# Kernel optimization log

Measured on AMD Instinct MI355X. Metric: run time of the kernel, lower is better.

## Reference

```python
import jax, jax.numpy as jnp
import numpy as np

B, L, C = 8, 4096, 1024
M = 16384  # memory bank size


def setup_inputs() -> dict:
    key = jax.random.key(0)
    k_f, k_w1, k_w2, k_mb = jax.random.split(key, 4)
    features = jax.random.normal(k_f, (B, L, C), dtype=jnp.float32)
    # Linear weights stored as (in, out); math identical to torch's x @ W.T + b.
    W1 = jax.random.normal(k_w1, (C, C // 2), dtype=jnp.float32) / np.sqrt(C)
    b1 = jnp.zeros((C // 2,), dtype=jnp.float32)
    W2 = jax.random.normal(k_w2, (C // 2, C // 4), dtype=jnp.float32) / np.sqrt(C // 2)
    b2 = jnp.zeros((C // 4,), dtype=jnp.float32)
    memory_bank = jax.random.normal(k_mb, (M, C // 4), dtype=jnp.float32)
    return {"features": features, "W1": W1, "b1": b1, "W2": W2, "b2": b2,
            "memory_bank": memory_bank}


def reference(features, W1, b1, W2, b2, memory_bank):
    # projection MLP: Linear -> ReLU -> Linear
    h = jax.nn.relu(jnp.einsum('blc,cd->bld', features, W1) + b1)
    proj = jnp.einsum('bld,de->ble', h, W2) + b2          # [B, L, D], D = C//4
    # Euclidean cdist against memory bank, then min over bank entries.
    x2 = jnp.sum(proj * proj, axis=-1, keepdims=True)      # [B, L, 1]
    m2 = jnp.sum(memory_bank * memory_bank, axis=-1)       # [M]
    xm = jnp.einsum('ble,me->blm', proj, memory_bank)      # [B, L, M]
    d2 = jnp.maximum(x2 - 2.0 * xm + m2, 0.0)
    dist = jnp.sqrt(d2)                                    # torch.cdist, p=2
    return jnp.min(dist, axis=-1)                          # [B, L]
```

## Files before the change

### kernel.cpp

```cpp
#include <hip/hip_runtime.h>
#include <math.h>

typedef __bf16 bf16;
typedef __attribute__((ext_vector_type(8))) __bf16 bf16x8;
typedef __attribute__((ext_vector_type(4))) float f32x4;
typedef __attribute__((ext_vector_type(8))) int i32x8;

typedef __attribute__((address_space(1))) const void gvoid;
typedef __attribute__((address_space(3))) void lvoid;
#define GLL(g, l) __builtin_amdgcn_global_load_lds((gvoid*)(g), (lvoid*)(l), 16, 0, 0)
#define MFMA(a, b, c) __builtin_amdgcn_mfma_f32_16x16x32_bf16((a), (b), (c), 0, 0, 0)
#define MFMAS(a, b, c) \
  __builtin_amdgcn_mfma_scale_f32_16x16x128_f8f6f4((a), (b), (c), 0, 0, 0, 0x7F, 0, 0x7F)

__device__ __forceinline__ int swz128(int row, int kb) { return kb ^ ((row & 7) << 4); }

__device__ __forceinline__ unsigned char f32_to_e4m3(float x) {
  const unsigned s = (__float_as_uint(x) >> 24) & 0x80;
  float ax = fminf(fabsf(x), 448.f);
  unsigned e;
  if (ax >= 0.015625f) {
    const unsigned u = __float_as_uint(ax);
    const unsigned t = u + 0x7FFFF + ((u >> 20) & 1);
    e = (((t >> 23) - 120) << 3) | ((t >> 20) & 7);
  } else {
    e = (unsigned)__float2int_rn(ax * 512.f);
  }
  return (unsigned char)(s | e);
}
__device__ __forceinline__ float e4m3_to_f32(unsigned char b) {
  const unsigned s = ((unsigned)b & 0x80) << 24;
  const unsigned em = b & 0x7F;
  float v;
  if (em >= 8) v = __uint_as_float((((em >> 3) + 120) << 23) | ((em & 7) << 20));
  else v = (float)em * 0.001953125f;
  return __uint_as_float(__float_as_uint(v) | s);
}

__global__ __launch_bounds__(256) void prep_w(const float* __restrict__ W1,
                                              const float* __restrict__ W2,
                                              bf16* __restrict__ W1t, bf16* __restrict__ W2t) {
  const int t = blockIdx.x * 256 + threadIdx.x;
  if (t < 512 * 1024) {
    const int h = t & 511, k = t >> 9;
    W1t[h * 1024 + k] = (bf16)W1[k * 512 + h];
  } else {
    const int u = t - 512 * 1024;
    const int e = u & 255, k = u >> 8;
    W2t[e * 512 + k] = (bf16)W2[k * 256 + e];
  }
}

__global__ __launch_bounds__(256) void prep_bank(const float* __restrict__ bank,
                                                 unsigned char* __restrict__ SB8,
                                                 float* __restrict__ m2) {
  const int tid = threadIdx.x, lane = tid & 63, wv = tid >> 6;
  const int row = blockIdx.x * 4 + wv;
  const float4 v = *reinterpret_cast<const float4*>(bank + (size_t)row * 256 + lane * 4);
  uchar4 q;
  float ssum = 0.f;
  {
    const float xs[4] = {v.x, v.y, v.z, v.w};
    unsigned char qb[4];
#pragma unroll
    for (int e = 0; e < 4; ++e) {
      qb[e] = f32_to_e4m3(-2.f * xs[e]);
      const float d = e4m3_to_f32(qb[e]);
      ssum += d * d;
    }
    q.x = qb[0]; q.y = qb[1]; q.z = qb[2]; q.w = qb[3];
  }
#pragma unroll
  for (int off = 1; off < 64; off <<= 1) ssum += __shfl_xor(ssum, off);
  const int t = row >> 7, ww = (row >> 4) & 7, lrr = row & 15;
  const int h = lane >> 5, lk = (lane >> 3) & 3, off32 = (lane & 7) * 4;
  const size_t dst = ((((size_t)t * 8 + ww) * 2 + h) * 64 + lk * 16 + lrr) * 32 + off32;
  *reinterpret_cast<uchar4*>(SB8 + dst) = q;
  if (lane == 0) m2[row] = ssum * 0.25f;
}

__global__ __launch_bounds__(512, 2) void mlp1_kernel(const float* __restrict__ F,
                                                      const bf16* __restrict__ W1t,
                                                      const float* __restrict__ b1,
                                                      bf16* __restrict__ H) {
  __shared__ __align__(16) char smem[81920];
  char* sA = smem;
  char* sB = smem + 16384;

  const int tid = threadIdx.x;
  const int w = tid >> 6, lane = tid & 63;
  const int wm = w >> 2, wn = w & 3;
  const int lr = lane & 15, lk = lane >> 4;
  const size_t r0 = (size_t)blockIdx.x * 128;

  f32x4 acc[4][8];
  const f32x4 z = {0.f, 0.f, 0.f, 0.f};
#pragma unroll
  for (int m = 0; m < 4; ++m)
#pragma unroll
    for (int n = 0; n < 8; ++n) acc[m][n] = z;

  for (int kc = 0; kc < 16; ++kc) {
    {
      const int fr = tid >> 2, kg = (tid & 3) << 4;
      const float* fsrc = F + (r0 + fr) * 1024 + kc * 64 + kg;
      const float4 f0 = *reinterpret_cast<const float4*>(fsrc);
      const float4 f1 = *reinterpret_cast<const float4*>(fsrc + 4);
      const float4 f2 = *reinterpret_cast<const float4*>(fsrc + 8);
      const float4 f3 = *reinterpret_cast<const float4*>(fsrc + 12);
      bf16x8 p0, p1;
      p0[0] = (bf16)f0.x; p0[1] = (bf16)f0.y; p0[2] = (bf16)f0.z; p0[3] = (bf16)f0.w;
      p0[4] = (bf16)f1.x; p0[5] = (bf16)f1.y; p0[6] = (bf16)f1.z; p0[7] = (bf16)f1.w;
      p1[0] = (bf16)f2.x; p1[1] = (bf16)f2.y; p1[2] = (bf16)f2.z; p1[3] = (bf16)f2.w;
      p1[4] = (bf16)f3.x; p1[5] = (bf16)f3.y; p1[6] = (bf16)f3.z; p1[7] = (bf16)f3.w;
      const int bb = kg * 2;
      *(bf16x8*)(sA + fr * 128 + swz128(fr, bb)) = p0;
      *(bf16x8*)(sA + fr * 128 + swz128(fr, bb + 16)) = p1;
    }
#pragma unroll
    for (int i = 0; i < 8; ++i) {
      const int o = (w * 8 + i) * 1024 + lane * 16;
      const int n = o >> 7, b = o & 127;
      GLL((const char*)W1t + n * 2048 + kc * 128 + swz128(n, b), sB + (w * 8 + i) * 1024);
    }
    __syncthreads();
#pragma unroll
    for (int ks = 0; ks < 2; ++ks) {
      bf16x8 av[4];
#pragma unroll
      for (int Mt = 0; Mt < 4; ++Mt) {
        const int row = wm * 64 + Mt * 16 + lr;
        av[Mt] = *(const bf16x8*)(sA + row * 128 + swz128(row, ks * 64 + lk * 16));
      }
#pragma unroll
      for (int Nt = 0; Nt < 8; ++Nt) {
        const int n = wn * 128 + Nt * 16 + lr;
        const bf16x8 bv = *(const bf16x8*)(sB + n * 128 + swz128(n, ks * 64 + lk * 16));
#pragma unroll
        for (int Mt = 0; Mt < 4; ++Mt) acc[Mt][Nt] = MFMA(av[Mt], bv, acc[Mt][Nt]);
      }
    }
    __syncthreads();
  }
#pragma unroll
  for (int Nt = 0; Nt < 8; ++Nt) {
    const int col = wn * 128 + Nt * 16 + lr;
    const float bias = b1[col];
#pragma unroll
    for (int Mt = 0; Mt < 4; ++Mt) {
      const size_t rowb = r0 + wm * 64 + Mt * 16 + lk * 4;
#pragma unroll
      for (int q = 0; q < 4; ++q)
        H[(rowb + q) * 512 + col] = (bf16)fmaxf(acc[Mt][Nt][q] + bias, 0.f);
    }
  }
}

__global__ __launch_bounds__(512, 2) void mlp2_kernel(const bf16* __restrict__ H,
                                                      const bf16* __restrict__ W2t,
                                                      const float* __restrict__ b2,
                                                      unsigned char* __restrict__ PROJ8,
                                                      float* __restrict__ X2) {
  __shared__ __align__(16) char smem[51200];
  char* sA = smem;
  char* sB = smem + 16384;
  float* sX2 = (float*)(smem + 49152);

  const int tid = threadIdx.x;
  const int w = tid >> 6, lane = tid & 63;
  const int wm = w >> 2, wn = w & 3;
  const int lr = lane & 15, lk = lane >> 4;
  const size_t r0 = (size_t)blockIdx.x * 128;

  f32x4 acc[4][4];
  const f32x4 z = {0.f, 0.f, 0.f, 0.f};
#pragma unroll
  for (int m = 0; m < 4; ++m)
#pragma unroll
    for (int n = 0; n < 4; ++n) acc[m][n] = z;

  for (int kc = 0; kc < 8; ++kc) {
#pragma unroll
    for (int i = 0; i < 2; ++i) {
      const int o = (w * 2 + i) * 1024 + lane * 16;
      const int row = o >> 7, b = o & 127;
      GLL((const char*)H + (r0 + row) * 1024 + kc * 128 + swz128(row, b), sA + (w * 2 + i) * 1024);
    }
#pragma unroll
    for (int i = 0; i < 4; ++i) {
      const int o = (w * 4 + i) * 1024 + lane * 16;
      const int n = o >> 7, b = o & 127;
      GLL((const char*)W2t + n * 1024 + kc * 128 + swz128(n, b), sB + (w * 4 + i) * 1024);
    }
    __syncthreads();
#pragma unroll
    for (int ks = 0; ks < 2; ++ks) {
      bf16x8 av[4];
#pragma unroll
      for (int Mt = 0; Mt < 4; ++Mt) {
        const int row = wm * 64 + Mt * 16 + lr;
        av[Mt] = *(const bf16x8*)(sA + row * 128 + swz128(row, ks * 64 + lk * 16));
      }
#pragma unroll
      for (int Nt = 0; Nt < 4; ++Nt) {
        const int n = wn * 64 + Nt * 16 + lr;
        const bf16x8 bv = *(const bf16x8*)(sB + n * 128 + swz128(n, ks * 64 + lk * 16));
#pragma unroll
        for (int Mt = 0; Mt < 4; ++Mt) acc[Mt][Nt] = MFMA(av[Mt], bv, acc[Mt][Nt]);
      }
    }
    __syncthreads();
  }
  float x2p[4][4];
#pragma unroll
  for (int m = 0; m < 4; ++m)
#pragma unroll
    for (int q = 0; q < 4; ++q) x2p[m][q] = 0.f;
#pragma unroll
  for (int Nt = 0; Nt < 4; ++Nt) {
    const int col = wn * 64 + Nt * 16 + lr;
    const float bias = b2[col];
#pragma unroll
    for (int Mt = 0; Mt < 4; ++Mt) {
      const size_t rowb = r0 + wm * 64 + Mt * 16 + lk * 4;
#pragma unroll
      for (int q = 0; q < 4; ++q) {
        const float p = acc[Mt][Nt][q] + bias;
        const unsigned char qb = f32_to_e4m3(p);
        PROJ8[(rowb + q) * 256 + col] = qb;
        const float d = e4m3_to_f32(qb);
        x2p[Mt][q] += d * d;
      }
    }
  }
#pragma unroll
  for (int Mt = 0; Mt < 4; ++Mt)
#pragma unroll
    for (int q = 0; q < 4; ++q) {
      float v = x2p[Mt][q];
      v += __shfl_xor(v, 1); v += __shfl_xor(v, 2);
      v += __shfl_xor(v, 4); v += __shfl_xor(v, 8);
      x2p[Mt][q] = v;
    }
  __syncthreads();
  if (lr == 0) {
#pragma unroll
    for (int Mt = 0; Mt < 4; ++Mt)
#pragma unroll
      for (int q = 0; q < 4; ++q)
        sX2[wn * 128 + wm * 64 + Mt * 16 + lk * 4 + q] = x2p[Mt][q];
  }
  __syncthreads();
  if (tid < 128)
    X2[r0 + tid] = sX2[tid] + sX2[128 + tid] + sX2[256 + tid] + sX2[384 + tid];
}

__global__ __launch_bounds__(512, 2) void dist_kernel(const unsigned char* __restrict__ PROJ8,
                                                      const unsigned char* __restrict__ SB8,
                                                      const float* __restrict__ m2g,
                                                      const float* __restrict__ X2,
                                                      float* __restrict__ out) {
  __shared__ float minbuf[1024];

  const int tid = threadIdx.x;
  const int w = tid >> 6, lane = tid & 63;
  const int lr = lane & 15, lk = lane >> 4;
  const size_t r0 = (size_t)blockIdx.x * 128;

  i32x8 A[8][2];
#pragma unroll
  for (int Mt = 0; Mt < 8; ++Mt)
#pragma unroll
    for (int h = 0; h < 2; ++h)
      A[Mt][h] = *(const i32x8*)(PROJ8 + (r0 + Mt * 16 + lr) * 256 + h * 128 + lk * 32);

  const char* sb = (const char*)SB8 + ((size_t)w * 2 * 64 + lane) * 32;
  const float* m2p = m2g + w * 16 + lr;

  f32x4 minv[8];
#pragma unroll
  for (int Mt = 0; Mt < 8; ++Mt)
#pragma unroll
    for (int q = 0; q < 4; ++q) minv[Mt][q] = 3.0e38f;

#define LOADT(B0, B1, MC, tt)                                \
  do {                                                       \
    B0 = *(const i32x8*)(sb + (size_t)(tt) * 32768);         \
    B1 = *(const i32x8*)(sb + (size_t)(tt) * 32768 + 2048);  \
    MC = m2p[(tt) * 128];                                    \
  } while (0)

#define COMPUTE(B0, B1, MC)                                                       \
  do {                                                                            \
    f32x4 mv;                                                                     \
    mv[0] = (MC); mv[1] = (MC); mv[2] = (MC); mv[3] = (MC);                       \
    f32x4 acc[8];                                                                 \
    __builtin_amdgcn_s_setprio(1);                                                \
    _Pragma("unroll") for (int Mt = 0; Mt < 8; ++Mt)                              \
      acc[Mt] = MFMAS(A[Mt][0], (B0), mv);                                        \
    _Pragma("unroll") for (int Mt = 0; Mt < 8; ++Mt)                              \
      acc[Mt] = MFMAS(A[Mt][1], (B1), acc[Mt]);                                   \
    __builtin_amdgcn_s_setprio(0);                                                \
    _Pragma("unroll") for (int Mt = 0; Mt < 8; ++Mt) {                            \
      minv[Mt][0] = fminf(minv[Mt][0], acc[Mt][0]);                               \
      minv[Mt][1] = fminf(minv[Mt][1], acc[Mt][1]);                               \
      minv[Mt][2] = fminf(minv[Mt][2], acc[Mt][2]);                               \
      minv[Mt][3] = fminf(minv[Mt][3], acc[Mt][3]);                               \
    }                                                                             \
  } while (0)

  i32x8 a0, a1, b0, b1;
  float ma, mb;
  LOADT(a0, a1, ma, 0);
  LOADT(b0, b1, mb, 1);

  for (int t = 0; t < 128; t += 2) {
    COMPUTE(a0, a1, ma);
    LOADT(a0, a1, ma, t + 2);
    COMPUTE(b0, b1, mb);
    LOADT(b0, b1, mb, t + 3);
  }
#undef LOADT
#undef COMPUTE

#pragma unroll
  for (int Mt = 0; Mt < 8; ++Mt)
#pragma unroll
    for (int q = 0; q < 4; ++q) {
      float v = minv[Mt][q];
      v = fminf(v, __shfl_xor(v, 1)); v = fminf(v, __shfl_xor(v, 2));
      v = fminf(v, __shfl_xor(v, 4)); v = fminf(v, __shfl_xor(v, 8));
      minv[Mt][q] = v;
    }
  if (lr == 0) {
#pragma unroll
    for (int Mt = 0; Mt < 8; ++Mt)
#pragma unroll
      for (int q = 0; q < 4; ++q)
        minbuf[w * 128 + Mt * 16 + lk * 4 + q] = minv[Mt][q];
  }
  __syncthreads();
  if (tid < 128) {
    float m = minbuf[tid];
#pragma unroll
    for (int v = 1; v < 8; ++v) m = fminf(m, minbuf[v * 128 + tid]);
    const float d2 = X2[r0 + tid] + m;
    out[r0 + tid] = sqrtf(fmaxf(d2, 0.f));
  }
}

extern "C" void kernel_launch(void* const* d_in, const int* in_sizes, int n_in,
                              void* d_out, int out_size, void* d_ws, size_t ws_size,
                              hipStream_t stream) {
  const float* F = (const float*)d_in[0];
  const float* W1 = (const float*)d_in[1];
  const float* b1 = (const float*)d_in[2];
  const float* W2 = (const float*)d_in[3];
  const float* b2 = (const float*)d_in[4];
  const float* bank = (const float*)d_in[5];
  float* out = (float*)d_out;

  char* ws = (char*)d_ws;
  unsigned char* SB8 = (unsigned char*)(ws + 0);
  float* m2 = (float*)(ws + 4325376);
  bf16* W1t = (bf16*)(ws + 4392960);
  bf16* W2t = (bf16*)(ws + 5441536);
  bf16* H = (bf16*)(ws + 5703680);
  unsigned char* PROJ8 = (unsigned char*)(ws + 39258112);
  float* X2 = (float*)(ws + 47646720);

  prep_w<<<2560, 256, 0, stream>>>(W1, W2, W1t, W2t);
  prep_bank<<<4096, 256, 0, stream>>>(bank, SB8, m2);
  mlp1_kernel<<<256, 512, 0, stream>>>(F, W1t, b1, H);
  mlp2_kernel<<<256, 512, 0, stream>>>(H, W2t, b2, PROJ8, X2);
  dist_kernel<<<256, 512, 0, stream>>>(PROJ8, SB8, m2, X2, out);
}
```

Measured before the change: 208.7 us.

## Switch distance kernel to 32x32x64 FP8 MFMA and merge prep kernels

The distance kernel now uses the 32x32x64 scaled FP8 MFMA instead of 16x16x128, with the bank layout rewritten in prep to match the new operand fragment. Each wave covers 64 rows by 32 bank entries per tile, and the cross-wave min reduction changes to match. The two prep kernels are merged into one launch to save a kernel launch. The larger MFMA shape raises operand reuse per instruction but uses more accumulator registers and needs wider shuffle reductions.

Measured after the change: 204.4 us. -2.1%, faster.

```diff
diff --git a/kernel.cpp b/kernel.cpp
--- a/kernel.cpp
+++ b/kernel.cpp
@@ -4,14 +4,15 @@
 typedef __bf16 bf16;
 typedef __attribute__((ext_vector_type(8))) __bf16 bf16x8;
 typedef __attribute__((ext_vector_type(4))) float f32x4;
+typedef __attribute__((ext_vector_type(16))) float f32x16;
 typedef __attribute__((ext_vector_type(8))) int i32x8;
 
 typedef __attribute__((address_space(1))) const void gvoid;
 typedef __attribute__((address_space(3))) void lvoid;
 #define GLL(g, l) __builtin_amdgcn_global_load_lds((gvoid*)(g), (lvoid*)(l), 16, 0, 0)
 #define MFMA(a, b, c) __builtin_amdgcn_mfma_f32_16x16x32_bf16((a), (b), (c), 0, 0, 0)
-#define MFMAS(a, b, c) \
-  __builtin_amdgcn_mfma_scale_f32_16x16x128_f8f6f4((a), (b), (c), 0, 0, 0, 0x7F, 0, 0x7F)
+#define MFMAS32(a, b, c) \
+  __builtin_amdgcn_mfma_scale_f32_32x32x64_f8f6f4((a), (b), (c), 0, 0, 0, 0x7F, 0, 0x7F)
 
 __device__ __forceinline__ int swz128(int row, int kb) { return kb ^ ((row & 7) << 4); }
 
@@ -37,25 +38,27 @@
   return __uint_as_float(__float_as_uint(v) | s);
 }
 
-__global__ __launch_bounds__(256) void prep_w(const float* __restrict__ W1,
-                                              const float* __restrict__ W2,
-                                              bf16* __restrict__ W1t, bf16* __restrict__ W2t) {
-  const int t = blockIdx.x * 256 + threadIdx.x;
-  if (t < 512 * 1024) {
-    const int h = t & 511, k = t >> 9;
-    W1t[h * 1024 + k] = (bf16)W1[k * 512 + h];
-  } else {
-    const int u = t - 512 * 1024;
-    const int e = u & 255, k = u >> 8;
-    W2t[e * 512 + k] = (bf16)W2[k * 256 + e];
-  }
-}
-
-__global__ __launch_bounds__(256) void prep_bank(const float* __restrict__ bank,
-                                                 unsigned char* __restrict__ SB8,
-                                                 float* __restrict__ m2) {
+__global__ __launch_bounds__(256) void prep_all(const float* __restrict__ W1,
+                                                const float* __restrict__ W2,
+                                                const float* __restrict__ bank,
+                                                bf16* __restrict__ W1t, bf16* __restrict__ W2t,
+                                                unsigned char* __restrict__ SB8,
+                                                float* __restrict__ m2) {
+  const int blk = blockIdx.x;
+  if (blk < 2560) {
+    const int t = blk * 256 + threadIdx.x;
+    if (t < 512 * 1024) {
+      const int h = t & 511, k = t >> 9;
+      W1t[h * 1024 + k] = (bf16)W1[k * 512 + h];
+    } else {
+      const int u = t - 512 * 1024;
+      const int e = u & 255, k = u >> 8;
+      W2t[e * 512 + k] = (bf16)W2[k * 256 + e];
+    }
+    return;
+  }
   const int tid = threadIdx.x, lane = tid & 63, wv = tid >> 6;
-  const int row = blockIdx.x * 4 + wv;
+  const int row = (blk - 2560) * 4 + wv;
   const float4 v = *reinterpret_cast<const float4*>(bank + (size_t)row * 256 + lane * 4);
   uchar4 q;
   float ssum = 0.f;
@@ -72,9 +75,10 @@
   }
 #pragma unroll
   for (int off = 1; off < 64; off <<= 1) ssum += __shfl_xor(ssum, off);
-  const int t = row >> 7, ww = (row >> 4) & 7, lrr = row & 15;
-  const int h = lane >> 5, lk = (lane >> 3) & 3, off32 = (lane & 7) * 4;
-  const size_t dst = ((((size_t)t * 8 + ww) * 2 + h) * 64 + lk * 16 + lrr) * 32 + off32;
+  const int k0 = lane * 4;
+  const int t = row >> 7, bg = (row >> 5) & 3, l31 = row & 31;
+  const int kc4 = k0 >> 6, hi = (k0 >> 5) & 1, j = k0 & 31;
+  const size_t dst = (size_t)((t * 4 + bg) * 4 + kc4) * 2048 + (hi * 32 + l31) * 32 + j;
   *reinterpret_cast<uchar4*>(SB8 + dst) = q;
   if (lane == 0) m2[row] = ssum * 0.25f;
 }
@@ -260,90 +264,89 @@
                                                       const float* __restrict__ m2g,
                                                       const float* __restrict__ X2,
                                                       float* __restrict__ out) {
-  __shared__ float minbuf[1024];
+  __shared__ float minbuf[512];
 
   const int tid = threadIdx.x;
   const int w = tid >> 6, lane = tid & 63;
-  const int lr = lane & 15, lk = lane >> 4;
+  const int l31 = lane & 31, hi = lane >> 5;
+  const int bg = w & 3, rh = w >> 2;
   const size_t r0 = (size_t)blockIdx.x * 128;
 
-  i32x8 A[8][2];
-#pragma unroll
-  for (int Mt = 0; Mt < 8; ++Mt)
-#pragma unroll
-    for (int h = 0; h < 2; ++h)
-      A[Mt][h] = *(const i32x8*)(PROJ8 + (r0 + Mt * 16 + lr) * 256 + h * 128 + lk * 32);
-
-  const char* sb = (const char*)SB8 + ((size_t)w * 2 * 64 + lane) * 32;
-  const float* m2p = m2g + w * 16 + lr;
-
-  f32x4 minv[8];
-#pragma unroll
-  for (int Mt = 0; Mt < 8; ++Mt)
-#pragma unroll
-    for (int q = 0; q < 4; ++q) minv[Mt][q] = 3.0e38f;
-
-#define LOADT(B0, B1, MC, tt)                                \
-  do {                                                       \
-    B0 = *(const i32x8*)(sb + (size_t)(tt) * 32768);         \
-    B1 = *(const i32x8*)(sb + (size_t)(tt) * 32768 + 2048);  \
-    MC = m2p[(tt) * 128];                                    \
+  i32x8 A[2][4];
+#pragma unroll
+  for (int rt = 0; rt < 2; ++rt)
+#pragma unroll
+    for (int kc = 0; kc < 4; ++kc)
+      A[rt][kc] =
+          *(const i32x8*)(PROJ8 + (r0 + rh * 64 + rt * 32 + l31) * 256 + kc * 64 + hi * 32);
+
+  const char* sb = (const char*)SB8 + (size_t)bg * 8192 + lane * 32;
+  const float* m2p = m2g + bg * 32 + l31;
+
+  f32x16 minv0, minv1;
+#pragma unroll
+  for (int r = 0; r < 16; ++r) { minv0[r] = 3.0e38f; minv1[r] = 3.0e38f; }
+
+#define LOADT(B, MC, tt)                                                \
+  do {                                                                  \
+    _Pragma("unroll") for (int kc = 0; kc < 4; ++kc)                    \
+      B[kc] = *(const i32x8*)(sb + (size_t)(tt) * 32768 + kc * 2048);   \
+    MC = m2p[(tt) * 128];                                               \
   } while (0)
 
-#define COMPUTE(B0, B1, MC)                                                       \
-  do {                                                                            \
-    f32x4 mv;                                                                     \
-    mv[0] = (MC); mv[1] = (MC); mv[2] = (MC); mv[3] = (MC);                       \
-    f32x4 acc[8];                                                                 \
-    __builtin_amdgcn_s_setprio(1);                                                \
-    _Pragma("unroll") for (int Mt = 0; Mt < 8; ++Mt)                              \
-      acc[Mt] = MFMAS(A[Mt][0], (B0), mv);                                        \
-    _Pragma("unroll") for (int Mt = 0; Mt < 8; ++Mt)                              \
-      acc[Mt] = MFMAS(A[Mt][1], (B1), acc[Mt]);                                   \
-    __builtin_amdgcn_s_setprio(0);                                                \
-    _Pragma("unroll") for (int Mt = 0; Mt < 8; ++Mt) {                            \
-      minv[Mt][0] = fminf(minv[Mt][0], acc[Mt][0]);                               \
-      minv[Mt][1] = fminf(minv[Mt][1], acc[Mt][1]);                               \
-      minv[Mt][2] = fminf(minv[Mt][2], acc[Mt][2]);                               \
-      minv[Mt][3] = fminf(minv[Mt][3], acc[Mt][3]);                               \
-    }                                                                             \
+#define COMPUTE(B, MC)                                                  \
+  do {                                                                  \
+    f32x16 acc0, acc1;                                                  \
+    _Pragma("unroll") for (int r = 0; r < 16; ++r) {                    \
+      acc0[r] = (MC); acc1[r] = (MC);                                   \
+    }                                                                   \
+    __builtin_amdgcn_s_setprio(1);                                      \
+    _Pragma("unroll") for (int kc = 0; kc < 4; ++kc) {                  \
+      acc0 = MFMAS32(A[0][kc], B[kc], acc0);                            \
+      acc1 = MFMAS32(A[1][kc], B[kc], acc1);                            \
+    }                                                                   \
+    __builtin_amdgcn_s_setprio(0);                                      \
+    _Pragma("unroll") for (int r = 0; r < 16; ++r) {                    \
+      minv0[r] = fminf(minv0[r], acc0[r]);                              \
+      minv1[r] = fminf(minv1[r], acc1[r]);                              \
+    }                                                                   \
   } while (0)
 
-  i32x8 a0, a1, b0, b1;
+  i32x8 Ba[4], Bb[4];
   float ma, mb;
-  LOADT(a0, a1, ma, 0);
-  LOADT(b0, b1, mb, 1);
+  LOADT(Ba, ma, 0);
 
   for (int t = 0; t < 128; t += 2) {
-    COMPUTE(a0, a1, ma);
-    LOADT(a0, a1, ma, t + 2);
-    COMPUTE(b0, b1, mb);
-    LOADT(b0, b1, mb, t + 3);
+    LOADT(Bb, mb, t + 1);
+    COMPUTE(Ba, ma);
+    LOADT(Ba, ma, t + 2);
+    COMPUTE(Bb, mb);
   }
 #undef LOADT
 #undef COMPUTE
 
 #pragma unroll
-  for (int Mt = 0; Mt < 8; ++Mt)
-#pragma unroll
-    for (int q = 0; q < 4; ++q) {
-      float v = minv[Mt][q];
-      v = fminf(v, __shfl_xor(v, 1)); v = fminf(v, __shfl_xor(v, 2));
-      v = fminf(v, __shfl_xor(v, 4)); v = fminf(v, __shfl_xor(v, 8));
-      minv[Mt][q] = v;
-    }
-  if (lr == 0) {
-#pragma unroll
-    for (int Mt = 0; Mt < 8; ++Mt)
-#pragma unroll
-      for (int q = 0; q < 4; ++q)
-        minbuf[w * 128 + Mt * 16 + lk * 4 + q] = minv[Mt][q];
+  for (int r = 0; r < 16; ++r) {
+    float v0 = minv0[r], v1 = minv1[r];
+#pragma unroll
+    for (int off = 1; off < 32; off <<= 1) {
+      v0 = fminf(v0, __shfl_xor(v0, off));
+      v1 = fminf(v1, __shfl_xor(v1, off));
+    }
+    minv0[r] = v0; minv1[r] = v1;
+  }
+  if (l31 == 0) {
+#pragma unroll
+    for (int r = 0; r < 16; ++r) {
+      const int rowa = (r & 3) + 8 * (r >> 2) + 4 * hi;
+      minbuf[bg * 128 + rh * 64 + rowa] = minv0[r];
+      minbuf[bg * 128 + rh * 64 + 32 + rowa] = minv1[r];
+    }
   }
   __syncthreads();
   if (tid < 128) {
-    float m = minbuf[tid];
-#pragma unroll
-    for (int v = 1; v < 8; ++v) m = fminf(m, minbuf[v * 128 + tid]);
+    const float m = fminf(fminf(minbuf[tid], minbuf[128 + tid]),
+                          fminf(minbuf[256 + tid], minbuf[384 + tid]));
     const float d2 = X2[r0 + tid] + m;
     out[r0 + tid] = sqrtf(fmaxf(d2, 0.f));
   }
@@ -369,8 +372,7 @@
   unsigned char* PROJ8 = (unsigned char*)(ws + 39258112);
   float* X2 = (float*)(ws + 47646720);
 
-  prep_w<<<2560, 256, 0, stream>>>(W1, W2, W1t, W2t);
-  prep_bank<<<4096, 256, 0, stream>>>(bank, SB8, m2);
+  prep_all<<<6656, 256, 0, stream>>>(W1, W2, bank, W1t, W2t, SB8, m2);
   mlp1_kernel<<<256, 512, 0, stream>>>(F, W1t, b1, H);
   mlp2_kernel<<<256, 512, 0, stream>>>(H, W2t, b2, PROJ8, X2);
   dist_kernel<<<256, 512, 0, stream>>>(PROJ8, SB8, m2, X2, out);
```
